# Kernel tuning notes

Hardware: AMD Instinct MI355X
Metric: run time of the kernel (lower is better)

Reference implementation:

```python
import jax, jax.numpy as jnp
import numpy as np

N = 100000   # nodes
E = 1600000  # edges (no self loops; module adds them)
D = 128      # in_dim == out_dim
BN_EPS = 1e-5
NORM_EPS = 1e-12


def setup_inputs() -> dict:
    key = jax.random.key(0)
    ks = jax.random.split(key, 9)
    x = jax.random.normal(ks[0], (N, D), jnp.float32)
    src = jax.random.randint(ks[1], (E,), 0, N, dtype=jnp.int32)
    dst = jax.random.randint(ks[2], (E,), 0, N, dtype=jnp.int32)
    dst = jnp.where(dst == src, (dst + 1) % N, dst)  # no pre-existing self loops
    edge_index = jnp.stack([src, dst], axis=0)
    edge_w = jax.random.uniform(ks[3], (E, 2), jnp.float32)
    # MySAGEConv.linear: Linear(2*D -> D) since concat=True
    W_lin = jax.random.normal(ks[4], (2 * D, D), jnp.float32) * (1.0 / np.sqrt(2 * D))
    b_lin = jnp.zeros((D,), jnp.float32)
    # BatchNorm1d(D)
    gamma = jnp.ones((D,), jnp.float32)
    beta = jnp.zeros((D,), jnp.float32)
    # PositionEmbedding(2, D): Linear(2->D//2, no bias), ReLU, Linear(D//2->D, no bias)
    pos_w1 = jax.random.normal(ks[5], (2, D // 2), jnp.float32) * 0.1
    pos_w2 = jax.random.normal(ks[6], (D // 2, D), jnp.float32) * 0.1
    return {"x": x, "edge_index": edge_index, "edge_w": edge_w,
            "W_lin": W_lin, "b_lin": b_lin, "gamma": gamma, "beta": beta,
            "pos_w1": pos_w1, "pos_w2": pos_w2}


def reference(x, edge_index, edge_w, W_lin, b_lin, gamma, beta, pos_w1, pos_w2):
    src, dst = edge_index[0], edge_index[1]
    # Position embedding is computed by the block but DISCARDED inside MySAGEConv.forward,
    # because add_remaining_self_loops(edge_index, None, 1, N) overwrites edge_weight with None.
    _pe = jnp.maximum(edge_w @ pos_w1, 0.0) @ pos_w2  # [E, D], unused (faithful to bug)
    # add_remaining_self_loops: append a self loop for every node
    loops = jnp.arange(N, dtype=src.dtype)
    src_f = jnp.concatenate([src, loops])
    dst_f = jnp.concatenate([dst, loops])
    # message = x_j (edge_weight is None); aggr = 'mean' scatter over destinations
    msg = x[src_f]                                           # [E+N, D] gather
    summed = jax.ops.segment_sum(msg, dst_f, num_segments=N)  # [N, D] scatter-add
    cnt = jax.ops.segment_sum(jnp.ones((E + N, 1), x.dtype), dst_f, num_segments=N)
    aggr = summed / cnt                                      # every node has >=1 (self loop)
    # update: concat + linear + L2 normalize
    h = jnp.concatenate([x, aggr], axis=-1) @ W_lin + b_lin   # [N, D]
    h = h / jnp.maximum(jnp.linalg.norm(h, axis=-1, keepdims=True), NORM_EPS)
    # BatchNorm1d (training-mode batch stats, biased variance)
    mu = jnp.mean(h, axis=0)
    var = jnp.var(h, axis=0)
    h = (h - mu) * jax.lax.rsqrt(var + BN_EPS) * gamma + beta
    # residual (in_dim == out_dim) + ReLU
    return jnp.maximum(h + x, 0.0)
```

## Files before the change

kernel.cpp:

```cpp
#include <hip/hip_runtime.h>
#include <hip/hip_bf16.h>

typedef __attribute__((ext_vector_type(4))) float f32x4;
typedef __attribute__((ext_vector_type(8))) short short8;
typedef __attribute__((ext_vector_type(4))) int i32x4;
typedef unsigned short u16;
typedef unsigned long long u64;

static __device__ __forceinline__ u16 f2bf(float f) {
    __hip_bfloat16 h = __float2bfloat16(f);
    return __builtin_bit_cast(u16, h);
}
static __device__ __forceinline__ float bf2f(u16 u) {
    unsigned int w = ((unsigned int)u) << 16;
    return __builtin_bit_cast(float, w);
}

__global__ void k_pre(const float* __restrict__ x, u16* __restrict__ xb, int total8,
                      const int* __restrict__ dst, int* __restrict__ deg,
                      int E, int chunk, int cvtBlocks) {
    int tid = threadIdx.x;
    if ((int)blockIdx.x < cvtBlocks) {
        const float4* x4 = (const float4*)x;
        int stride = cvtBlocks * 256;
        for (int i = blockIdx.x * 256 + tid; i < total8; i += stride) {
            float4 a = x4[i * 2], b = x4[i * 2 + 1];
            union { u16 u[8]; short8 v; } o;
            o.u[0] = f2bf(a.x); o.u[1] = f2bf(a.y); o.u[2] = f2bf(a.z); o.u[3] = f2bf(a.w);
            o.u[4] = f2bf(b.x); o.u[5] = f2bf(b.y); o.u[6] = f2bf(b.z); o.u[7] = f2bf(b.w);
            *(short8*)(xb + (size_t)i * 8) = o.v;
        }
    } else {
        int group = blockIdx.x & 7;
        int bseq = (blockIdx.x - cvtBlocks) >> 3;
        int nblk = (gridDim.x - cvtBlocks) >> 3;
        int lo = group * chunk, hi = lo + chunk;
        int E4 = E >> 2;
        const int4* d4 = (const int4*)dst;
        int stride = nblk * 256;
        int gid = bseq * 256 + tid;
        for (int i = gid; i < E4; i += stride) {
            int4 v = d4[i];
            if (v.x >= lo && v.x < hi) atomicAdd(&deg[v.x], 1);
            if (v.y >= lo && v.y < hi) atomicAdd(&deg[v.y], 1);
            if (v.z >= lo && v.z < hi) atomicAdd(&deg[v.z], 1);
            if (v.w >= lo && v.w < hi) atomicAdd(&deg[v.w], 1);
        }
        if (group == 0) {
            for (int e = E4 * 4 + gid; e < E; e += stride)
                atomicAdd(&deg[dst[e]], 1);
        }
    }
}

__global__ void k_scan_a(const int* __restrict__ deg, int* __restrict__ bsum, int n) {
    __shared__ int s[256];
    int tid = threadIdx.x;
    int i = blockIdx.x * 256 + tid;
    s[tid] = (i < n) ? deg[i] : 0;
    __syncthreads();
    for (int ofs = 128; ofs > 0; ofs >>= 1) {
        if (tid < ofs) s[tid] += s[tid + ofs];
        __syncthreads();
    }
    if (tid == 0) bsum[blockIdx.x] = s[0];
}

__global__ void k_scan_b(const int* __restrict__ bsum, int* __restrict__ boff, int nb,
                         int* __restrict__ offN) {
    __shared__ int s[512];
    int tid = threadIdx.x;
    int v = (tid < nb) ? bsum[tid] : 0;
    s[tid] = v;
    __syncthreads();
    for (int ofs = 1; ofs < 512; ofs <<= 1) {
        int t = (tid >= ofs) ? s[tid - ofs] : 0;
        __syncthreads();
        s[tid] += t;
        __syncthreads();
    }
    if (tid < nb) boff[tid] = s[tid] - v;
    if (tid == nb - 1) offN[0] = s[tid];
}

__global__ void k_scan_c(const int* __restrict__ deg, const int* __restrict__ boff,
                         int* __restrict__ off, int* __restrict__ cur, int n) {
    __shared__ int s[256];
    int tid = threadIdx.x;
    int i = blockIdx.x * 256 + tid;
    int v = (i < n) ? deg[i] : 0;
    s[tid] = v;
    __syncthreads();
    for (int ofs = 1; ofs < 256; ofs <<= 1) {
        int t = (tid >= ofs) ? s[tid - ofs] : 0;
        __syncthreads();
        s[tid] += t;
        __syncthreads();
    }
    int excl = s[tid] - v + boff[blockIdx.x];
    if (i < n) { off[i] = excl; cur[i] = excl; }
}

__global__ void k_fill(const int* __restrict__ src, const int* __restrict__ dst,
                       int* __restrict__ cur, int* __restrict__ csr, int E, int chunk) {
    const int NX = 8;
    int group = blockIdx.x & (NX - 1);
    int bseq = blockIdx.x >> 3;
    int nblk = gridDim.x >> 3;
    int lo = group * chunk, hi = lo + chunk;
    int E4 = E >> 2;
    const int4* d4 = (const int4*)dst;
    int stride = nblk * blockDim.x;
    int gid = bseq * blockDim.x + threadIdx.x;
    for (int i = gid; i < E4; i += stride) {
        int4 v = d4[i];
        int e = i * 4;
        if (v.x >= lo && v.x < hi) { int p = atomicAdd(&cur[v.x], 1); csr[p] = src[e]; }
        if (v.y >= lo && v.y < hi) { int p = atomicAdd(&cur[v.y], 1); csr[p] = src[e + 1]; }
        if (v.z >= lo && v.z < hi) { int p = atomicAdd(&cur[v.z], 1); csr[p] = src[e + 2]; }
        if (v.w >= lo && v.w < hi) { int p = atomicAdd(&cur[v.w], 1); csr[p] = src[e + 3]; }
    }
    if (group == 0) {
        for (int e = E4 * 4 + gid; e < E; e += stride) {
            int d = dst[e];
            int p = atomicAdd(&cur[d], 1);
            csr[p] = src[e];
        }
    }
}

__global__ void k_aggr(const u16* __restrict__ xb, const int* __restrict__ off,
                       const int* __restrict__ csr, u16* __restrict__ aggr, int n) {
    int node = (blockIdx.x * blockDim.x + threadIdx.x) >> 6;
    if (node >= n) return;
    int lane = threadIdx.x & 63;
    int c = lane & 15;
    int j = lane >> 4;
    const short8* x8 = (const short8*)xb;
    int s0 = off[node], s1 = off[node + 1];
    float acc[8] = {0.f, 0.f, 0.f, 0.f, 0.f, 0.f, 0.f, 0.f};
    int e = s0;
    for (; e + 16 <= s1; e += 16) {
        int r0 = csr[e + j], r1 = csr[e + j + 4], r2 = csr[e + j + 8], r3 = csr[e + j + 12];
        short8 v0 = x8[(size_t)r0 * 16 + c];
        short8 v1 = x8[(size_t)r1 * 16 + c];
        short8 v2 = x8[(size_t)r2 * 16 + c];
        short8 v3 = x8[(size_t)r3 * 16 + c];
#pragma unroll
        for (int i = 0; i < 8; ++i)
            acc[i] += (bf2f((u16)v0[i]) + bf2f((u16)v1[i])) +
                      (bf2f((u16)v2[i]) + bf2f((u16)v3[i]));
    }
    for (int r = e + j; r < s1; r += 4) {
        short8 v = x8[(size_t)csr[r] * 16 + c];
#pragma unroll
        for (int i = 0; i < 8; ++i) acc[i] += bf2f((u16)v[i]);
    }
#pragma unroll
    for (int i = 0; i < 8; ++i) {
        acc[i] += __shfl_xor(acc[i], 16, 64);
        acc[i] += __shfl_xor(acc[i], 32, 64);
    }
    if (j == 0) {
        short8 sv = x8[(size_t)node * 16 + c];
        float inv = 1.0f / (float)(s1 - s0 + 1);
        short8 o;
#pragma unroll
        for (int i = 0; i < 8; ++i)
            o[i] = (short)f2bf((acc[i] + bf2f((u16)sv[i])) * inv);
        *(short8*)(aggr + (size_t)node * 128 + c * 8) = o;
    }
}

__global__ __launch_bounds__(512, 2) void k_linear(
    const u16* __restrict__ xb, u16* __restrict__ aggr ,
    const float* __restrict__ W, const float* __restrict__ b_lin,
    float* __restrict__ bnsum, float* __restrict__ bnsq,
    int n, int ntiles) {
    __shared__ u16 WT[32768];
    int tid = threadIdx.x;

    {
        int col = tid & 127;
        int kq0 = tid >> 7;
        int mask = (col & 15) << 3;
        char* base = (char*)WT + col * 512;
#pragma unroll
        for (int i = 0; i < 16; ++i) {
            int kq = kq0 + i * 4;
            int k = kq * 4;
            float w0 = W[(size_t)(k + 0) * 128 + col];
            float w1 = W[(size_t)(k + 1) * 128 + col];
            float w2 = W[(size_t)(k + 2) * 128 + col];
            float w3 = W[(size_t)(k + 3) * 128 + col];
            u64 q = (u64)f2bf(w0) | ((u64)f2bf(w1) << 16) |
                    ((u64)f2bf(w2) << 32) | ((u64)f2bf(w3) << 48);
            *(u64*)(base + ((8 * kq) ^ mask)) = q;
        }
    }
    __syncthreads();

    int wave = tid >> 6, l = tid & 63, lr = l & 15, lg = l >> 4;
    int pair = wave >> 1, hf = wave & 1;

    short8 breg[4][8];
#pragma unroll
    for (int ct2 = 0; ct2 < 4; ++ct2) {
        int col = hf * 64 + ct2 * 16 + lr;
        const char* rowp = (const char*)WT + col * 512;
        int mask = (col & 15) << 3;
#pragma unroll
        for (int kk = 0; kk < 8; ++kk) {
            int kb = kk * 64 + 8 * lg;
            u64 lo = *(const u64*)(rowp + (kb ^ mask));
            u64 hi = *(const u64*)(rowp + ((kb + 32) ^ mask));
            union { u64 q[2]; short8 v; } bu;
            bu.q[0] = lo; bu.q[1] = hi;
            breg[ct2][kk] = bu.v;
        }
    }
    __syncthreads();
    float* ssx = (float*)WT;

    float s1a[4] = {0, 0, 0, 0};
    float s2a[4] = {0, 0, 0, 0};
    int stride4 = gridDim.x * 4;

    for (int base = blockIdx.x * 4; base < ntiles; base += stride4) {
        int tile = base + pair;
        bool active = tile < ntiles;
        int rowA = tile * 16 + lr;
        bool rv = active && rowA < n;

        ushort4 xa[4], xc[4], ua[4], ub[4];
#pragma unroll
        for (int kk = 0; kk < 4; ++kk) {
            const u16* xp = xb + (size_t)rowA * 128 + kk * 32 + 4 * lg;
            xa[kk] = rv ? *(const ushort4*)xp : make_ushort4(0, 0, 0, 0);
            xc[kk] = rv ? *(const ushort4*)(xp + 16) : make_ushort4(0, 0, 0, 0);
        }
#pragma unroll
        for (int kk = 0; kk < 4; ++kk) {
            const u16* ap = aggr + (size_t)rowA * 128 + kk * 32 + 4 * lg;
            ua[kk] = rv ? *(const ushort4*)ap : make_ushort4(0, 0, 0, 0);
            ub[kk] = rv ? *(const ushort4*)(ap + 16) : make_ushort4(0, 0, 0, 0);
        }

        short8 av[8];
#pragma unroll
        for (int kk = 0; kk < 4; ++kk) {
            av[kk][0] = (short)xa[kk].x; av[kk][1] = (short)xa[kk].y;
            av[kk][2] = (short)xa[kk].z; av[kk][3] = (short)xa[kk].w;
            av[kk][4] = (short)xc[kk].x; av[kk][5] = (short)xc[kk].y;
            av[kk][6] = (short)xc[kk].z; av[kk][7] = (short)xc[kk].w;
            av[kk + 4][0] = (short)ua[kk].x; av[kk + 4][1] = (short)ua[kk].y;
            av[kk + 4][2] = (short)ua[kk].z; av[kk + 4][3] = (short)ua[kk].w;
            av[kk + 4][4] = (short)ub[kk].x; av[kk + 4][5] = (short)ub[kk].y;
            av[kk + 4][6] = (short)ub[kk].z; av[kk + 4][7] = (short)ub[kk].w;
        }

        f32x4 acc[4];
#pragma unroll
        for (int ct2 = 0; ct2 < 4; ++ct2) acc[ct2] = (f32x4){0.f, 0.f, 0.f, 0.f};
#pragma unroll
        for (int kk = 0; kk < 8; ++kk)
#pragma unroll
            for (int ct2 = 0; ct2 < 4; ++ct2)
                acc[ct2] = __builtin_amdgcn_mfma_f32_16x16x32_bf16(av[kk], breg[ct2][kk],
                                                                   acc[ct2], 0, 0, 0);

        float ss[4] = {0.f, 0.f, 0.f, 0.f};
#pragma unroll
        for (int ct2 = 0; ct2 < 4; ++ct2) {
            float bl = b_lin[hf * 64 + ct2 * 16 + lr];
#pragma unroll
            for (int q = 0; q < 4; ++q) {
                acc[ct2][q] += bl;
                ss[q] += acc[ct2][q] * acc[ct2][q];
            }
        }
#pragma unroll
        for (int m = 1; m < 16; m <<= 1) {
#pragma unroll
            for (int q = 0; q < 4; ++q) ss[q] += __shfl_xor(ss[q], m, 64);
        }
        if (lr == 0)
            *(float4*)&ssx[(pair * 2 + hf) * 16 + lg * 4] =
                make_float4(ss[0], ss[1], ss[2], ss[3]);
        __syncthreads();
        float4 oth = *(const float4*)&ssx[(pair * 2 + (1 - hf)) * 16 + lg * 4];
        float sc[4];
        sc[0] = 1.0f / fmaxf(sqrtf(ss[0] + oth.x), 1e-12f);
        sc[1] = 1.0f / fmaxf(sqrtf(ss[1] + oth.y), 1e-12f);
        sc[2] = 1.0f / fmaxf(sqrtf(ss[2] + oth.z), 1e-12f);
        sc[3] = 1.0f / fmaxf(sqrtf(ss[3] + oth.w), 1e-12f);
        __syncthreads();

        if (active) {
            int rq0 = tile * 16 + 4 * lg;
#pragma unroll
            for (int ct2 = 0; ct2 < 4; ++ct2) {
                float hn[4];
                float p1 = 0.f, p2 = 0.f;
#pragma unroll
                for (int q = 0; q < 4; ++q) {
                    hn[q] = acc[ct2][q] * sc[q];
                    if (rq0 + q >= n) hn[q] = 0.f;
                    p1 += hn[q]; p2 += hn[q] * hn[q];
                }
                s1a[ct2] += p1; s2a[ct2] += p2;
                ushort4 o;
                o.x = f2bf(hn[0]); o.y = f2bf(hn[1]); o.z = f2bf(hn[2]); o.w = f2bf(hn[3]);
                *(ushort4*)(aggr + (size_t)tile * 2048 + (hf * 4 + ct2) * 256 + l * 4) = o;
            }
        }
    }

#pragma unroll
    for (int ct2 = 0; ct2 < 4; ++ct2) {
        float v1 = s1a[ct2], v2 = s2a[ct2];
        v1 += __shfl_xor(v1, 16, 64); v1 += __shfl_xor(v1, 32, 64);
        v2 += __shfl_xor(v2, 16, 64); v2 += __shfl_xor(v2, 32, 64);
        if (lg == 0) {
            atomicAdd(&bnsum[hf * 64 + ct2 * 16 + lr], v1);
            atomicAdd(&bnsq[hf * 64 + ct2 * 16 + lr], v2);
        }
    }
}

__global__ __launch_bounds__(512) void k_final(
    const u16* __restrict__ hfrag, const float* __restrict__ x,
    const float* __restrict__ bnsum, const float* __restrict__ bnsq,
    const float* __restrict__ gamma, const float* __restrict__ beta,
    float* __restrict__ out, float invN, int n) {
    __shared__ float cf[256];
    __shared__ float ot[16 * 132];
    int tid = threadIdx.x;
    int tile = blockIdx.x;
    if (tid < 128) {
        float mu = bnsum[tid] * invN;
        float var = bnsq[tid] * invN - mu * mu;
        float a = gamma[tid] * rsqrtf(var + 1e-5f);
        cf[tid] = a;
        cf[128 + tid] = beta[tid] - mu * a;
    }
    __syncthreads();

    {
        int ct = tid >> 6, l = tid & 63;
        ushort4 hv = *(const ushort4*)(hfrag + (size_t)tile * 2048 + ct * 256 + l * 4);
        int col = ct * 16 + (l & 15);
        float a = cf[col], b = cf[128 + col];
        int rl0 = 4 * (l >> 4);
        ot[(rl0 + 0) * 132 + col] = bf2f(hv.x) * a + b;
        ot[(rl0 + 1) * 132 + col] = bf2f(hv.y) * a + b;
        ot[(rl0 + 2) * 132 + col] = bf2f(hv.z) * a + b;
        ot[(rl0 + 3) * 132 + col] = bf2f(hv.w) * a + b;
    }
    __syncthreads();

    {
        int rl = tid >> 5, c4 = tid & 31;
        int row = tile * 16 + rl;
        if (row < n) {
            float4 xv = *(const float4*)(x + (size_t)row * 128 + c4 * 4);
            const float* op = &ot[rl * 132 + c4 * 4];
            float4 o;
            o.x = fmaxf(op[0] + xv.x, 0.f);
            o.y = fmaxf(op[1] + xv.y, 0.f);
            o.z = fmaxf(op[2] + xv.z, 0.f);
            o.w = fmaxf(op[3] + xv.w, 0.f);
            *(float4*)(out + (size_t)row * 128 + c4 * 4) = o;
        }
    }
}

extern "C" void kernel_launch(void* const* d_in, const int* in_sizes, int n_in,
                              void* d_out, int out_size, void* d_ws, size_t ws_size,
                              hipStream_t stream) {
    const float* x     = (const float*)d_in[0];
    const int*   ei    = (const int*)d_in[1];
    const float* W     = (const float*)d_in[3];
    const float* b_lin = (const float*)d_in[4];
    const float* gamma = (const float*)d_in[5];
    const float* beta  = (const float*)d_in[6];
    int N = in_sizes[0] / 128;
    int E = in_sizes[1] / 2;
    const int* src = ei;
    const int* dst = ei + E;

    char* p = (char*)d_ws;
    auto alloc = [&](size_t bytes) { char* r = p; p += (bytes + 255) & ~(size_t)255; return r; };
    int*   deg   = (int*)alloc((size_t)N * 4);
    float* bnsum = (float*)alloc(128 * 4);
    float* bnsq  = (float*)alloc(128 * 4);
    size_t zspan = (char*)(bnsq + 128) - (char*)deg;
    int*   off   = (int*)alloc((size_t)(N + 1) * 4);
    int*   cur   = (int*)alloc((size_t)N * 4);
    int*   csr   = (int*)alloc((size_t)E * 4);
    int*   bsum  = (int*)alloc(512 * 4);
    int*   boff  = (int*)alloc(512 * 4);
    u16*   aggr  = (u16*)alloc((size_t)N * 128 * 2);

    u16* xbf = (u16*)d_out;

    hipMemsetAsync(deg, 0, zspan, stream);

    const int NGROUP = 8;
    int chunk = (N + NGROUP - 1) / NGROUP;
    const int CVTB = 768;

    k_pre<<<CVTB + 1024, 256, 0, stream>>>(x, xbf, N * 16, dst, deg, E, chunk, CVTB);
    int nb = (N + 255) / 256;
    k_scan_a<<<nb, 256, 0, stream>>>(deg, bsum, N);
    k_scan_b<<<1, 512, 0, stream>>>(bsum, boff, nb, off + N);
    k_scan_c<<<nb, 256, 0, stream>>>(deg, boff, off, cur, N);
    k_fill<<<1024, 256, 0, stream>>>(src, dst, cur, csr, E, chunk);
    k_aggr<<<(int)(((size_t)N * 64 + 255) / 256), 256, 0, stream>>>(xbf, off, csr, aggr, N);
    int ntiles = (N + 15) / 16;
    k_linear<<<512, 512, 0, stream>>>(xbf, aggr, W, b_lin, bnsum, bnsq, N, ntiles);
    k_final<<<ntiles, 512, 0, stream>>>(aggr, x, bnsum, bnsq, gamma, beta,
                                        (float*)d_out, 1.0f / (float)N, N);
}
```

Baseline: 310.2 us.

## Remove per-tile block syncs in linear kernel by deferring row-norm scaling

The linear kernel no longer exchanges half-row squared sums through shared memory with two __syncthreads per tile. Instead it writes per-row partial sums to a global buffer and stores unnormalized bf16 outputs into the upper half of the output buffer. A second pass computes the BN statistics from normalized values, and the final kernel applies the row normalization itself. It also reads fp32 x directly instead of the bf16 copy, and halves the grid to 256 blocks. The cost is an extra global read pass over h, plus in-place aliasing of the output buffer, which is safe only if tile writes never overlap unread data.

```diff
diff --git a/kernel.cpp b/kernel.cpp
--- a/kernel.cpp
+++ b/kernel.cpp
@@ -3,7 +3,6 @@
 
 typedef __attribute__((ext_vector_type(4))) float f32x4;
 typedef __attribute__((ext_vector_type(8))) short short8;
-typedef __attribute__((ext_vector_type(4))) int i32x4;
 typedef unsigned short u16;
 typedef unsigned long long u64;
 
@@ -173,10 +172,11 @@
 }
 
 __global__ __launch_bounds__(512, 2) void k_linear(
-    const u16* __restrict__ xb, u16* __restrict__ aggr ,
+    const float* __restrict__ x, const u16* __restrict__ aggr,
     const float* __restrict__ W, const float* __restrict__ b_lin,
-    float* __restrict__ bnsum, float* __restrict__ bnsq,
-    int n, int ntiles) {
+    u16* __restrict__ hout ,
+    float* __restrict__ ssp, float* __restrict__ bnsum, float* __restrict__ bnsq,
+    int n, int ntiles, int npad) {
     __shared__ u16 WT[32768];
     int tid = threadIdx.x;
 
@@ -219,11 +219,7 @@
             breg[ct2][kk] = bu.v;
         }
     }
-    __syncthreads();
-    float* ssx = (float*)WT;
-
-    float s1a[4] = {0, 0, 0, 0};
-    float s2a[4] = {0, 0, 0, 0};
+
     int stride4 = gridDim.x * 4;
 
     for (int base = blockIdx.x * 4; base < ntiles; base += stride4) {
@@ -232,12 +228,15 @@
         int rowA = tile * 16 + lr;
         bool rv = active && rowA < n;
 
-        ushort4 xa[4], xc[4], ua[4], ub[4];
+        float4 xa[4], xc[4];
+        ushort4 ua[4], ub[4];
 #pragma unroll
         for (int kk = 0; kk < 4; ++kk) {
-            const u16* xp = xb + (size_t)rowA * 128 + kk * 32 + 4 * lg;
-            xa[kk] = rv ? *(const ushort4*)xp : make_ushort4(0, 0, 0, 0);
-            xc[kk] = rv ? *(const ushort4*)(xp + 16) : make_ushort4(0, 0, 0, 0);
+            int k1 = kk * 32 + 4 * lg;
+            xa[kk] = rv ? *(const float4*)(x + (size_t)rowA * 128 + k1)
+                        : make_float4(0.f, 0.f, 0.f, 0.f);
+            xc[kk] = rv ? *(const float4*)(x + (size_t)rowA * 128 + k1 + 16)
+                        : make_float4(0.f, 0.f, 0.f, 0.f);
         }
 #pragma unroll
         for (int kk = 0; kk < 4; ++kk) {
@@ -249,10 +248,10 @@
         short8 av[8];
 #pragma unroll
         for (int kk = 0; kk < 4; ++kk) {
-            av[kk][0] = (short)xa[kk].x; av[kk][1] = (short)xa[kk].y;
-            av[kk][2] = (short)xa[kk].z; av[kk][3] = (short)xa[kk].w;
-            av[kk][4] = (short)xc[kk].x; av[kk][5] = (short)xc[kk].y;
-            av[kk][6] = (short)xc[kk].z; av[kk][7] = (short)xc[kk].w;
+            av[kk][0] = (short)f2bf(xa[kk].x); av[kk][1] = (short)f2bf(xa[kk].y);
+            av[kk][2] = (short)f2bf(xa[kk].z); av[kk][3] = (short)f2bf(xa[kk].w);
+            av[kk][4] = (short)f2bf(xc[kk].x); av[kk][5] = (short)f2bf(xc[kk].y);
+            av[kk][6] = (short)f2bf(xc[kk].z); av[kk][7] = (short)f2bf(xc[kk].w);
             av[kk + 4][0] = (short)ua[kk].x; av[kk + 4][1] = (short)ua[kk].y;
             av[kk + 4][2] = (short)ua[kk].z; av[kk + 4][3] = (short)ua[kk].w;
             av[kk + 4][4] = (short)ub[kk].x; av[kk + 4][5] = (short)ub[kk].y;
@@ -284,35 +283,47 @@
 #pragma unroll
             for (int q = 0; q < 4; ++q) ss[q] += __shfl_xor(ss[q], m, 64);
         }
-        if (lr == 0)
-            *(float4*)&ssx[(pair * 2 + hf) * 16 + lg * 4] =
-                make_float4(ss[0], ss[1], ss[2], ss[3]);
-        __syncthreads();
-        float4 oth = *(const float4*)&ssx[(pair * 2 + (1 - hf)) * 16 + lg * 4];
-        float sc[4];
-        sc[0] = 1.0f / fmaxf(sqrtf(ss[0] + oth.x), 1e-12f);
-        sc[1] = 1.0f / fmaxf(sqrtf(ss[1] + oth.y), 1e-12f);
-        sc[2] = 1.0f / fmaxf(sqrtf(ss[2] + oth.z), 1e-12f);
-        sc[3] = 1.0f / fmaxf(sqrtf(ss[3] + oth.w), 1e-12f);
-        __syncthreads();
-
         if (active) {
             int rq0 = tile * 16 + 4 * lg;
+            if (lr == 0)
+                *(float4*)&ssp[hf * npad + rq0] = make_float4(ss[0], ss[1], ss[2], ss[3]);
+            u16* hp = hout + (size_t)tile * 4096 + 2048;
 #pragma unroll
             for (int ct2 = 0; ct2 < 4; ++ct2) {
-                float hn[4];
-                float p1 = 0.f, p2 = 0.f;
-#pragma unroll
-                for (int q = 0; q < 4; ++q) {
-                    hn[q] = acc[ct2][q] * sc[q];
-                    if (rq0 + q >= n) hn[q] = 0.f;
-                    p1 += hn[q]; p2 += hn[q] * hn[q];
-                }
-                s1a[ct2] += p1; s2a[ct2] += p2;
                 ushort4 o;
-                o.x = f2bf(hn[0]); o.y = f2bf(hn[1]); o.z = f2bf(hn[2]); o.w = f2bf(hn[3]);
-                *(ushort4*)(aggr + (size_t)tile * 2048 + (hf * 4 + ct2) * 256 + l * 4) = o;
+                o.x = f2bf(acc[ct2][0]); o.y = f2bf(acc[ct2][1]);
+                o.z = f2bf(acc[ct2][2]); o.w = f2bf(acc[ct2][3]);
+                *(ushort4*)(hp + (hf * 4 + ct2) * 256 + l * 4) = o;
             }
+        }
+    }
+
+    __syncthreads();
+
+    float s1a[4] = {0, 0, 0, 0};
+    float s2a[4] = {0, 0, 0, 0};
+    for (int base = blockIdx.x * 4; base < ntiles; base += stride4) {
+        int tile = base + pair;
+        if (tile >= ntiles) continue;
+        int rq0 = tile * 16 + 4 * lg;
+        float rn[4];
+#pragma unroll
+        for (int q = 0; q < 4; ++q) {
+            float s2 = ssp[rq0 + q] + ssp[npad + rq0 + q];
+            rn[q] = 1.0f / fmaxf(sqrtf(s2), 1e-12f);
+        }
+        const u16* hp = hout + (size_t)tile * 4096 + 2048;
+#pragma unroll
+        for (int ct2 = 0; ct2 < 4; ++ct2) {
+            ushort4 hv = *(const ushort4*)(hp + (hf * 4 + ct2) * 256 + l * 4);
+            float p1 = 0.f, p2 = 0.f;
+            float h0 = bf2f(hv.x) * rn[0], h1 = bf2f(hv.y) * rn[1];
+            float h2 = bf2f(hv.z) * rn[2], h3 = bf2f(hv.w) * rn[3];
+            if (rq0 + 0 < n) { p1 += h0; p2 += h0 * h0; }
+            if (rq0 + 1 < n) { p1 += h1; p2 += h1 * h1; }
+            if (rq0 + 2 < n) { p1 += h2; p2 += h2 * h2; }
+            if (rq0 + 3 < n) { p1 += h3; p2 += h3 * h3; }
+            s1a[ct2] += p1; s2a[ct2] += p2;
         }
     }
 
@@ -329,10 +340,10 @@
 }
 
 __global__ __launch_bounds__(512) void k_final(
-    const u16* __restrict__ hfrag, const float* __restrict__ x,
+    const float* __restrict__ ssp, const float* __restrict__ x,
     const float* __restrict__ bnsum, const float* __restrict__ bnsq,
     const float* __restrict__ gamma, const float* __restrict__ beta,
-    float* __restrict__ out, float invN, int n) {
+    float* __restrict__ out, float invN, int n, int npad) {
     __shared__ float cf[256];
     __shared__ float ot[16 * 132];
     int tid = threadIdx.x;
@@ -347,15 +358,21 @@
     __syncthreads();
 
     {
+        const u16* hp = (const u16*)out + (size_t)tile * 4096 + 2048;
         int ct = tid >> 6, l = tid & 63;
-        ushort4 hv = *(const ushort4*)(hfrag + (size_t)tile * 2048 + ct * 256 + l * 4);
+        ushort4 hv = *(const ushort4*)(hp + ct * 256 + l * 4);
         int col = ct * 16 + (l & 15);
         float a = cf[col], b = cf[128 + col];
         int rl0 = 4 * (l >> 4);
-        ot[(rl0 + 0) * 132 + col] = bf2f(hv.x) * a + b;
-        ot[(rl0 + 1) * 132 + col] = bf2f(hv.y) * a + b;
-        ot[(rl0 + 2) * 132 + col] = bf2f(hv.z) * a + b;
-        ot[(rl0 + 3) * 132 + col] = bf2f(hv.w) * a + b;
+        int rq0 = tile * 16 + rl0;
+        float rn0 = 1.0f / fmaxf(sqrtf(ssp[rq0 + 0] + ssp[npad + rq0 + 0]), 1e-12f);
+        float rn1 = 1.0f / fmaxf(sqrtf(ssp[rq0 + 1] + ssp[npad + rq0 + 1]), 1e-12f);
+        float rn2 = 1.0f / fmaxf(sqrtf(ssp[rq0 + 2] + ssp[npad + rq0 + 2]), 1e-12f);
+        float rn3 = 1.0f / fmaxf(sqrtf(ssp[rq0 + 3] + ssp[npad + rq0 + 3]), 1e-12f);
+        ot[(rl0 + 0) * 132 + col] = bf2f(hv.x) * rn0 * a + b;
+        ot[(rl0 + 1) * 132 + col] = bf2f(hv.y) * rn1 * a + b;
+        ot[(rl0 + 2) * 132 + col] = bf2f(hv.z) * rn2 * a + b;
+        ot[(rl0 + 3) * 132 + col] = bf2f(hv.w) * rn3 * a + b;
     }
     __syncthreads();
 
@@ -389,6 +406,9 @@
     const int* src = ei;
     const int* dst = ei + E;
 
+    int ntiles = (N + 15) / 16;
+    int npad = ntiles * 16;
+
     char* p = (char*)d_ws;
     auto alloc = [&](size_t bytes) { char* r = p; p += (bytes + 255) & ~(size_t)255; return r; };
     int*   deg   = (int*)alloc((size_t)N * 4);
@@ -400,6 +420,7 @@
     int*   csr   = (int*)alloc((size_t)E * 4);
     int*   bsum  = (int*)alloc(512 * 4);
     int*   boff  = (int*)alloc(512 * 4);
+    float* ssp   = (float*)alloc((size_t)npad * 2 * 4);
     u16*   aggr  = (u16*)alloc((size_t)N * 128 * 2);
 
     u16* xbf = (u16*)d_out;
@@ -417,8 +438,8 @@
     k_scan_c<<<nb, 256, 0, stream>>>(deg, boff, off, cur, N);
     k_fill<<<1024, 256, 0, stream>>>(src, dst, cur, csr, E, chunk);
     k_aggr<<<(int)(((size_t)N * 64 + 255) / 256), 256, 0, stream>>>(xbf, off, csr, aggr, N);
-    int ntiles = (N + 15) / 16;
-    k_linear<<<512, 512, 0, stream>>>(xbf, aggr, W, b_lin, bnsum, bnsq, N, ntiles);
-    k_final<<<ntiles, 512, 0, stream>>>(aggr, x, bnsum, bnsq, gamma, beta,
-                                        (float*)d_out, 1.0f / (float)N, N);
-}
+    k_linear<<<256, 512, 0, stream>>>(x, aggr, W, b_lin, (u16*)d_out, ssp,
+                                      bnsum, bnsq, N, ntiles, npad);
+    k_final<<<ntiles, 512, 0, stream>>>(ssp, x, bnsum, bnsq, gamma, beta,
+                                        (float*)d_out, 1.0f / (float)N, N, npad);
+}
```

Measured after the change: 297.3 us. -4.1%, faster.
